# Kernel optimization log

Hardware: AMD Instinct MI355X
Metric: run time of the kernel (lower is better)

## Reference

```python
import jax, jax.numpy as jnp
import numpy as np

S = 14
STEP = 1.0 / S
LAMBDA_COORD = 7.0
LAMBDA_NOOBJ = 0.2
LAMBDA_CLS = 1.5
EPS = 1e-06


def _abs_coords(boxes):
    # boxes: [N, S, S, 2, 5] -> [N, S, S, 2, 4] (x1,y1,x2,y2)
    ys, xs = jnp.meshgrid(jnp.arange(S, dtype=boxes.dtype), jnp.arange(S, dtype=boxes.dtype), indexing='ij')
    xg = xs[None, :, :, None]
    yg = ys[None, :, :, None]
    cx = (boxes[..., 0] + xg) * STEP
    cy = (boxes[..., 1] + yg) * STEP
    w = boxes[..., 2]
    h = boxes[..., 3]
    return jnp.stack([cx - w / 2, cy - h / 2, cx + w / 2, cy + h / 2], axis=-1)


def _iou(b1, b2):
    x1 = jnp.maximum(b1[..., 0], b2[..., 0])
    y1 = jnp.maximum(b1[..., 1], b2[..., 1])
    x2 = jnp.minimum(b1[..., 2], b2[..., 2])
    y2 = jnp.minimum(b1[..., 3], b2[..., 3])
    inter = jnp.clip(x2 - x1, 0) * jnp.clip(y2 - y1, 0)
    a1 = (b1[..., 2] - b1[..., 0]) * (b1[..., 3] - b1[..., 1])
    a2 = (b2[..., 2] - b2[..., 0]) * (b2[..., 3] - b2[..., 1])
    return inter / (a1 + a2 - inter + EPS)


def _ciou_loss(b1, b2):
    iou = _iou(b1, b2)
    cx1 = (b1[..., 0] + b1[..., 2]) / 2
    cy1 = (b1[..., 1] + b1[..., 3]) / 2
    cx2 = (b2[..., 0] + b2[..., 2]) / 2
    cy2 = (b2[..., 1] + b2[..., 3]) / 2
    center_dist = (cx1 - cx2) ** 2 + (cy1 - cy2) ** 2
    xc1 = jnp.minimum(b1[..., 0], b2[..., 0])
    yc1 = jnp.minimum(b1[..., 1], b2[..., 1])
    xc2 = jnp.maximum(b1[..., 2], b2[..., 2])
    yc2 = jnp.maximum(b1[..., 3], b2[..., 3])
    outer_diag = (xc2 - xc1) ** 2 + (yc2 - yc1) ** 2 + EPS
    w1 = jnp.clip(b1[..., 2] - b1[..., 0], EPS)
    h1 = jnp.clip(b1[..., 3] - b1[..., 1], EPS)
    w2 = jnp.clip(b2[..., 2] - b2[..., 0], EPS)
    h2 = jnp.clip(b2[..., 3] - b2[..., 1], EPS)
    v = (4.0 / jnp.pi ** 2) * (jnp.arctan(w2 / h2) - jnp.arctan(w1 / h1)) ** 2
    alpha = v / (1 - iou + v + EPS)
    ciou = iou - center_dist / outer_diag - alpha * v
    scale = jnp.clip(2 - w2 * h2, 1.0)
    return (1 - ciou) * scale


def setup_inputs() -> dict:
    key = jax.random.key(0)
    k1, k2 = jax.random.split(key)
    N = 4096
    pred = jax.random.uniform(k1, (N, S, S, 30), dtype=jnp.float32)
    target = jax.random.uniform(k2, (N, S, S, 30), dtype=jnp.float32)
    return {"pred": pred, "target": target}


def reference(pred, target):
    N = pred.shape[0]
    tb = target[..., :10].reshape(N, S, S, 2, 5)
    pb = pred[..., :10].reshape(N, S, S, 2, 5)
    tcls = target[..., 10:]
    pcls = pred[..., 10:]

    obj = tb[..., 4] > 0                      # [N,S,S,2]
    pabs = _abs_coords(pb)                    # [N,S,S,2,4]
    tabs = _abs_coords(tb)

    # responsible-box assignment: IoU of both pred boxes vs target box 0
    ious = _iou(pabs, tabs[..., 0:1, :])      # [N,S,S,2]
    max_i = jnp.argmax(ious, axis=-1)         # first-max tie-break, same as torch
    resp = max_i[..., None] == jnp.arange(2)  # [N,S,S,2] bool
    obj = obj & resp
    noobj = ~obj

    pconf = pb[..., 4]
    tconf = tb[..., 4]
    se = (pconf - tconf) ** 2
    noobj_loss = jnp.sum(se * noobj)
    obj_loss = jnp.sum(se * obj)

    bbox_loss = jnp.sum(_ciou_loss(pabs, tabs) * obj)

    sig = jnp.any(obj, axis=-1)               # [N,S,S]
    # torch F.binary_cross_entropy clamps log terms at -100
    logp = jnp.clip(jnp.log(pcls), -100.0)
    log1mp = jnp.clip(jnp.log1p(-pcls), -100.0)
    bce = -(tcls * logp + (1 - tcls) * log1mp)
    class_loss = jnp.sum(bce * sig[..., None]) * LAMBDA_CLS

    loss = obj_loss + LAMBDA_NOOBJ * noobj_loss + LAMBDA_COORD * bbox_loss + class_loss
    return loss / N
```

## Files before the change

kernel.cpp:

```cpp
#include <hip/hip_runtime.h>
#include <math.h>

namespace {
constexpr int SG = 14;
constexpr int NIMG = 4096;
constexpr int NCELLS = NIMG * SG * SG;
constexpr int CPB = 256;
constexpr int PAD = 31;
constexpr float STEPF = 1.0f / 14.0f;
constexpr float EPSF = 1e-6f;
constexpr float L_COORD = 7.0f;
constexpr float L_NOOBJ = 0.2f;
constexpr float L_CLS = 1.5f;
constexpr float INV_N = 1.0f / 4096.0f;
constexpr float FOUR_OVER_PI2 = 4.0f / (float)(M_PI * M_PI);
}

struct Box { float x1, y1, x2, y2; };

__device__ __forceinline__ float iou_fn(const Box& a, const Box& b) {
  float ix1 = fmaxf(a.x1, b.x1);
  float iy1 = fmaxf(a.y1, b.y1);
  float ix2 = fminf(a.x2, b.x2);
  float iy2 = fminf(a.y2, b.y2);
  float inter = fmaxf(ix2 - ix1, 0.0f) * fmaxf(iy2 - iy1, 0.0f);
  float a1 = (a.x2 - a.x1) * (a.y2 - a.y1);
  float a2 = (b.x2 - b.x1) * (b.y2 - b.y1);
  return __fdividef(inter, a1 + a2 - inter + EPSF);
}

__global__ __launch_bounds__(256) void yolo_loss_kernel(
    const float* __restrict__ pred, const float* __restrict__ tgt,
    float* __restrict__ out) {
  __shared__ float buf[CPB * PAD];
  __shared__ float sdata[4];

  const int tid = threadIdx.x;

  {
    const float2* P2 = reinterpret_cast<const float2*>(pred) + (size_t)blockIdx.x * (CPB * 15);
#pragma unroll
    for (int j = 0; j < 15; ++j) {
      const int idx = j * 256 + tid;
      const int c = idx / 15;
      const int addr = 2 * idx + c;
      const float2 v = P2[idx];
      buf[addr] = v.x; buf[addr + 1] = v.y;
    }
  }
  __syncthreads();

  float p[30];
#pragma unroll
  for (int k = 0; k < 30; ++k) p[k] = buf[tid * PAD + k];
  __syncthreads();

  {
    const float2* T2 = reinterpret_cast<const float2*>(tgt) + (size_t)blockIdx.x * (CPB * 15);
#pragma unroll
    for (int j = 0; j < 15; ++j) {
      const int idx = j * 256 + tid;
      const int c = idx / 15;
      const int addr = 2 * idx + c;
      const float2 u = T2[idx];
      buf[addr] = u.x; buf[addr + 1] = u.y;
    }
  }
  __syncthreads();

  float tb[10];
#pragma unroll
  for (int k = 0; k < 10; ++k) tb[k] = buf[tid * PAD + k];

  const int cell = blockIdx.x * CPB + tid;
  const int rem = cell % (SG * SG);
  const float gx = (float)(rem % SG);
  const float gy = (float)(rem / SG);

  Box pa0, pa1, ta0, ta1;
  {
    float cx = (p[0] + gx) * STEPF, cy = (p[1] + gy) * STEPF, w = p[2], h = p[3];
    pa0 = {cx - 0.5f * w, cy - 0.5f * h, cx + 0.5f * w, cy + 0.5f * h};
    cx = (p[5] + gx) * STEPF; cy = (p[6] + gy) * STEPF; w = p[7]; h = p[8];
    pa1 = {cx - 0.5f * w, cy - 0.5f * h, cx + 0.5f * w, cy + 0.5f * h};
    cx = (tb[0] + gx) * STEPF; cy = (tb[1] + gy) * STEPF; w = tb[2]; h = tb[3];
    ta0 = {cx - 0.5f * w, cy - 0.5f * h, cx + 0.5f * w, cy + 0.5f * h};
    cx = (tb[5] + gx) * STEPF; cy = (tb[6] + gy) * STEPF; w = tb[7]; h = tb[8];
    ta1 = {cx - 0.5f * w, cy - 0.5f * h, cx + 0.5f * w, cy + 0.5f * h};
  }

  const float iou0 = iou_fn(pa0, ta0);
  const float iou1 = iou_fn(pa1, ta0);
  const bool m1 = iou1 > iou0;
  const bool obj0 = (tb[4] > 0.0f) && !m1;
  const bool obj1 = (tb[9] > 0.0f) && m1;
  const bool sig = obj0 || obj1;

  const float d0 = p[4] - tb[4], d1 = p[9] - tb[9];
  const float se0 = d0 * d0, se1 = d1 * d1;
  const float obj_loss   = (obj0 ? se0 : 0.0f) + (obj1 ? se1 : 0.0f);
  const float noobj_loss = (obj0 ? 0.0f : se0) + (obj1 ? 0.0f : se1);

  Box b1, b2;
  b1.x1 = m1 ? pa1.x1 : pa0.x1; b1.y1 = m1 ? pa1.y1 : pa0.y1;
  b1.x2 = m1 ? pa1.x2 : pa0.x2; b1.y2 = m1 ? pa1.y2 : pa0.y2;
  b2.x1 = m1 ? ta1.x1 : ta0.x1; b2.y1 = m1 ? ta1.y1 : ta0.y1;
  b2.x2 = m1 ? ta1.x2 : ta0.x2; b2.y2 = m1 ? ta1.y2 : ta0.y2;

  float bbox;
  {
    const float iou = iou_fn(b1, b2);
    const float cx1 = 0.5f * (b1.x1 + b1.x2), cy1 = 0.5f * (b1.y1 + b1.y2);
    const float cx2 = 0.5f * (b2.x1 + b2.x2), cy2 = 0.5f * (b2.y1 + b2.y2);
    const float cd = (cx1 - cx2) * (cx1 - cx2) + (cy1 - cy2) * (cy1 - cy2);
    const float ox1 = fminf(b1.x1, b2.x1), oy1 = fminf(b1.y1, b2.y1);
    const float ox2 = fmaxf(b1.x2, b2.x2), oy2 = fmaxf(b1.y2, b2.y2);
    const float od = (ox2 - ox1) * (ox2 - ox1) + (oy2 - oy1) * (oy2 - oy1) + EPSF;
    const float w1 = fmaxf(b1.x2 - b1.x1, EPSF), h1 = fmaxf(b1.y2 - b1.y1, EPSF);
    const float w2 = fmaxf(b2.x2 - b2.x1, EPSF), h2 = fmaxf(b2.y2 - b2.y1, EPSF);
    const float dat = atanf(__fdividef(w2, h2)) - atanf(__fdividef(w1, h1));
    const float v = FOUR_OVER_PI2 * dat * dat;
    const float alpha = __fdividef(v, 1.0f - iou + v + EPSF);
    const float ciou = iou - __fdividef(cd, od) - alpha * v;
    const float scale = fmaxf(2.0f - w2 * h2, 1.0f);
    bbox = sig ? (1.0f - ciou) * scale : 0.0f;
  }

  float cls = 0.0f;
#pragma unroll
  for (int k = 0; k < 20; ++k) {
    const float pc = p[10 + k];
    const float tc = buf[tid * PAD + 10 + k];
    const float lg   = fmaxf(__logf(pc), -100.0f);
    const float l1mp = fmaxf(__logf(1.0f - pc), -100.0f);
    cls += -(tc * lg + (1.0f - tc) * l1mp);
  }

  float acc = obj_loss + L_NOOBJ * noobj_loss + L_COORD * bbox
            + (sig ? L_CLS * cls : 0.0f);

#pragma unroll
  for (int off = 32; off > 0; off >>= 1) acc += __shfl_down(acc, off);

  const int lane = tid & 63;
  const int wid  = tid >> 6;
  if (lane == 0) sdata[wid] = acc;
  __syncthreads();
  if (tid == 0) {
    const float s = sdata[0] + sdata[1] + sdata[2] + sdata[3];
    atomicAdd(out, s * INV_N);
  }
}

extern "C" void kernel_launch(void* const* d_in, const int* in_sizes, int n_in,
                              void* d_out, int out_size, void* d_ws, size_t ws_size,
                              hipStream_t stream) {
  const float* pred = (const float*)d_in[0];
  const float* tgt  = (const float*)d_in[1];
  float* out = (float*)d_out;

  hipMemsetAsync(out, 0, sizeof(float), stream);

  const int blocks = NCELLS / CPB;
  yolo_loss_kernel<<<blocks, CPB, 0, stream>>>(pred, tgt, out);
}
```

Measured before the change: 207.6 us.

## Issue all pred/target loads up front and compute BCE in coalesced layout

Loads both pred and target float2 chunks into registers at the same time, so all global loads are in flight together instead of being split into two phases by a barrier. Only the 10 box fields per cell are staged in shared memory. The 20 class BCE terms are computed directly in the coalesced load layout and summed per cell with shared-memory atomics. Shared memory per block shrinks and the launch bounds now request 6 blocks per CU, at the cost of 60 live load registers per thread and contended LDS atomics.

```diff
diff --git a/kernel.cpp b/kernel.cpp
--- a/kernel.cpp
+++ b/kernel.cpp
@@ -6,7 +6,7 @@
 constexpr int NIMG = 4096;
 constexpr int NCELLS = NIMG * SG * SG;
 constexpr int CPB = 256;
-constexpr int PAD = 31;
+constexpr int STRIDE = 11;
 constexpr float STEPF = 1.0f / 14.0f;
 constexpr float EPSF = 1e-6f;
 constexpr float L_COORD = 7.0f;
@@ -29,48 +29,57 @@
   return __fdividef(inter, a1 + a2 - inter + EPSF);
 }
 
-__global__ __launch_bounds__(256) void yolo_loss_kernel(
+__device__ __forceinline__ float bce_term(float pc, float tc) {
+  const float lg   = fmaxf(__logf(pc), -100.0f);
+  const float l1mp = fmaxf(__logf(1.0f - pc), -100.0f);
+  return -(tc * lg + (1.0f - tc) * l1mp);
+}
+
+__global__ __launch_bounds__(256, 6) void yolo_loss_kernel(
     const float* __restrict__ pred, const float* __restrict__ tgt,
     float* __restrict__ out) {
-  __shared__ float buf[CPB * PAD];
+  __shared__ float bp[CPB * STRIDE];
+  __shared__ float bt[CPB * STRIDE];
+  __shared__ float bce[CPB];
   __shared__ float sdata[4];
 
   const int tid = threadIdx.x;
 
-  {
-    const float2* P2 = reinterpret_cast<const float2*>(pred) + (size_t)blockIdx.x * (CPB * 15);
+  const float2* P2 = reinterpret_cast<const float2*>(pred) + (size_t)blockIdx.x * (CPB * 15);
+  const float2* T2 = reinterpret_cast<const float2*>(tgt)  + (size_t)blockIdx.x * (CPB * 15);
+  float2 pv[15], tv[15];
 #pragma unroll
-    for (int j = 0; j < 15; ++j) {
-      const int idx = j * 256 + tid;
-      const int c = idx / 15;
-      const int addr = 2 * idx + c;
-      const float2 v = P2[idx];
-      buf[addr] = v.x; buf[addr + 1] = v.y;
+  for (int j = 0; j < 15; ++j) {
+    pv[j] = P2[j * 256 + tid];
+    tv[j] = T2[j * 256 + tid];
+  }
+
+  bce[tid] = 0.0f;
+  __syncthreads();
+
+#pragma unroll
+  for (int j = 0; j < 15; ++j) {
+    const int idx = j * 256 + tid;
+    const int c = idx / 15;
+    const int e = 2 * idx - 30 * c;
+    const float2 v = pv[j];
+    const float2 u = tv[j];
+    if (e < 10) {
+      bp[c * STRIDE + e] = v.x; bp[c * STRIDE + e + 1] = v.y;
+      bt[c * STRIDE + e] = u.x; bt[c * STRIDE + e + 1] = u.y;
+    } else {
+      const float s = bce_term(v.x, u.x) + bce_term(v.y, u.y);
+      atomicAdd(&bce[c], s);
     }
   }
   __syncthreads();
 
-  float p[30];
+  float p[10], t[10];
 #pragma unroll
-  for (int k = 0; k < 30; ++k) p[k] = buf[tid * PAD + k];
-  __syncthreads();
-
-  {
-    const float2* T2 = reinterpret_cast<const float2*>(tgt) + (size_t)blockIdx.x * (CPB * 15);
-#pragma unroll
-    for (int j = 0; j < 15; ++j) {
-      const int idx = j * 256 + tid;
-      const int c = idx / 15;
-      const int addr = 2 * idx + c;
-      const float2 u = T2[idx];
-      buf[addr] = u.x; buf[addr + 1] = u.y;
-    }
+  for (int k = 0; k < 10; ++k) {
+    p[k] = bp[tid * STRIDE + k];
+    t[k] = bt[tid * STRIDE + k];
   }
-  __syncthreads();
-
-  float tb[10];
-#pragma unroll
-  for (int k = 0; k < 10; ++k) tb[k] = buf[tid * PAD + k];
 
   const int cell = blockIdx.x * CPB + tid;
   const int rem = cell % (SG * SG);
@@ -83,20 +92,20 @@
     pa0 = {cx - 0.5f * w, cy - 0.5f * h, cx + 0.5f * w, cy + 0.5f * h};
     cx = (p[5] + gx) * STEPF; cy = (p[6] + gy) * STEPF; w = p[7]; h = p[8];
     pa1 = {cx - 0.5f * w, cy - 0.5f * h, cx + 0.5f * w, cy + 0.5f * h};
-    cx = (tb[0] + gx) * STEPF; cy = (tb[1] + gy) * STEPF; w = tb[2]; h = tb[3];
+    cx = (t[0] + gx) * STEPF; cy = (t[1] + gy) * STEPF; w = t[2]; h = t[3];
     ta0 = {cx - 0.5f * w, cy - 0.5f * h, cx + 0.5f * w, cy + 0.5f * h};
-    cx = (tb[5] + gx) * STEPF; cy = (tb[6] + gy) * STEPF; w = tb[7]; h = tb[8];
+    cx = (t[5] + gx) * STEPF; cy = (t[6] + gy) * STEPF; w = t[7]; h = t[8];
     ta1 = {cx - 0.5f * w, cy - 0.5f * h, cx + 0.5f * w, cy + 0.5f * h};
   }
 
   const float iou0 = iou_fn(pa0, ta0);
   const float iou1 = iou_fn(pa1, ta0);
   const bool m1 = iou1 > iou0;
-  const bool obj0 = (tb[4] > 0.0f) && !m1;
-  const bool obj1 = (tb[9] > 0.0f) && m1;
+  const bool obj0 = (t[4] > 0.0f) && !m1;
+  const bool obj1 = (t[9] > 0.0f) && m1;
   const bool sig = obj0 || obj1;
 
-  const float d0 = p[4] - tb[4], d1 = p[9] - tb[9];
+  const float d0 = p[4] - t[4], d1 = p[9] - t[9];
   const float se0 = d0 * d0, se1 = d1 * d1;
   const float obj_loss   = (obj0 ? se0 : 0.0f) + (obj1 ? se1 : 0.0f);
   const float noobj_loss = (obj0 ? 0.0f : se0) + (obj1 ? 0.0f : se1);
@@ -126,18 +135,8 @@
     bbox = sig ? (1.0f - ciou) * scale : 0.0f;
   }
 
-  float cls = 0.0f;
-#pragma unroll
-  for (int k = 0; k < 20; ++k) {
-    const float pc = p[10 + k];
-    const float tc = buf[tid * PAD + 10 + k];
-    const float lg   = fmaxf(__logf(pc), -100.0f);
-    const float l1mp = fmaxf(__logf(1.0f - pc), -100.0f);
-    cls += -(tc * lg + (1.0f - tc) * l1mp);
-  }
-
   float acc = obj_loss + L_NOOBJ * noobj_loss + L_COORD * bbox
-            + (sig ? L_CLS * cls : 0.0f);
+            + (sig ? L_CLS * bce[tid] : 0.0f);
 
 #pragma unroll
   for (int off = 32; off > 0; off >>= 1) acc += __shfl_down(acc, off);
@@ -159,7 +158,7 @@
   const float* tgt  = (const float*)d_in[1];
   float* out = (float*)d_out;
 
-  hipMemsetAsync(out, 0, sizeof(float), stream);
+  hipMemsetAsync(out, 0, (size_t)out_size * sizeof(float), stream);
 
   const int blocks = NCELLS / CPB;
   yolo_loss_kernel<<<blocks, CPB, 0, stream>>>(pred, tgt, out);
```

Result: slower. 218.5 us (+5.3%).
